# Kernel optimization log

Hardware: AMD Instinct MI355X
Metric: run time of the kernel (lower is better)

Reference implementation:

```python
import jax, jax.numpy as jnp
import numpy as np

NUM_BINS = 8
TAIL = 3.0
MBW = 1e-3  # min_bin_width
MBH = 1e-3  # min_bin_height
MD = 1e-3   # min_derivative
B, C, H, W = 16, 12, 128, 128
COND = C // 3
HID = 64
STEP = 3 * NUM_BINS - 1
OUT = C * STEP


def setup_inputs() -> dict:
    key = jax.random.key(0)
    ks = jax.random.split(key, 8)
    s = lambda k, shape, scale=1.0: jax.random.normal(k, shape, jnp.float32) * scale
    return {
        'x': s(ks[0], (B, C, H, W)),
        'logdet': jnp.zeros((B,), jnp.float32),
        'conditioning': s(ks[1], (B, COND, H, W)),
        'W1': s(ks[2], (HID, C + COND, 3, 3), 0.05), 'b1': jnp.zeros((HID,), jnp.float32),
        'W2': s(ks[3], (HID, HID, 1, 1), 0.05), 'b2': jnp.zeros((HID,), jnp.float32),
        'W3': s(ks[4], (OUT, HID, 3, 3), 0.05), 'b3': jnp.zeros((OUT,), jnp.float32),
    }


def _conv(x, w, b, pad):
    y = jax.lax.conv_general_dilated(x, w, (1, 1), [(pad, pad), (pad, pad)],
                                     dimension_numbers=('NCHW', 'OIHW', 'NCHW'))
    return y + b[None, :, None, None]


def _checker_mask(h, w, parity):
    ii, jj = jnp.meshgrid(jnp.arange(h), jnp.arange(w), indexing='ij')
    m = jnp.where((ii + jj) % 2 == 0, parity, 1 - parity)
    return m.astype(jnp.float32)[None, None]  # (1,1,H,W)


def _rqs_forward(x, uw, uh, ud):
    # x: (B,C,H,W); uw/uh: (...,K); ud: (...,K-1). 'linear' tails, tail_bound=TAIL.
    K = NUM_BINS
    left, right = -TAIL, TAIL
    inside = (x >= left) & (x <= right)
    xc = jnp.clip(x, left, right)

    w = MBW + (1.0 - MBW * K) * jax.nn.softmax(uw, axis=-1)
    cw = jnp.pad(jnp.cumsum(w, -1), [(0, 0)] * (w.ndim - 1) + [(1, 0)])
    cw = (right - left) * cw + left
    cw = cw.at[..., 0].set(left).at[..., -1].set(right)
    w = cw[..., 1:] - cw[..., :-1]

    h = MBH + (1.0 - MBH * K) * jax.nn.softmax(uh, axis=-1)
    ch = jnp.pad(jnp.cumsum(h, -1), [(0, 0)] * (h.ndim - 1) + [(1, 0)])
    ch = (right - left) * ch + left
    ch = ch.at[..., 0].set(left).at[..., -1].set(right)
    h = ch[..., 1:] - ch[..., :-1]

    const = float(np.log(np.expm1(1.0 - MD)))  # boundary derivative -> 1 under linear tails
    udp = jnp.pad(ud, [(0, 0)] * (ud.ndim - 1) + [(1, 1)], constant_values=const)
    d = MD + jax.nn.softplus(udp)  # (...,K+1)

    delta = h / w
    # searchsorted: bin index per element
    idx = jnp.clip(jnp.sum((xc[..., None] >= cw).astype(jnp.int32), -1) - 1, 0, K - 1)[..., None]
    g = lambda t: jnp.take_along_axis(t, idx, axis=-1)[..., 0]

    icw, iw = g(cw), g(w)
    ich, ih = g(ch), g(h)
    idl = g(delta)
    id0 = g(d)
    id1 = g(d[..., 1:])

    theta = (xc - icw) / iw
    t1 = theta * (1.0 - theta)
    num = ih * (idl * theta ** 2 + id0 * t1)
    den = idl + (id0 + id1 - 2.0 * idl) * t1
    y = ich + num / den
    dnum = idl ** 2 * (id1 * theta ** 2 + 2.0 * idl * t1 + id0 * (1.0 - theta) ** 2)
    lad = jnp.log(dnum) - 2.0 * jnp.log(den)
    return jnp.where(inside, y, x), jnp.where(inside, lad, 0.0)


def reference(x, logdet, conditioning, W1, b1, W2, b2, W3, b3):
    mask = _checker_mask(H, W, 0)
    x_frozen = mask * x
    x_active = (1.0 - mask) * x
    z = jnp.concatenate([x_frozen, conditioning], axis=1)
    h1 = jax.nn.relu(_conv(z, W1, b1, 1))
    h2 = jax.nn.relu(_conv(h1, W2, b2, 0))
    params = _conv(h2, W3, b3, 1)  # (B, C*STEP, H, W)
    # all channels at once instead of python loop over C
    p = params.reshape(B, C, STEP, H, W).transpose(0, 1, 3, 4, 2)  # (B,C,H,W,STEP)
    uw = p[..., :NUM_BINS]
    uh = p[..., NUM_BINS:2 * NUM_BINS]
    ud = p[..., 2 * NUM_BINS:]
    y, lad = _rqs_forward(x_active, uw, uh, ud)
    x_out = x_frozen + y  # matches original: frozen part + spline output (no re-masking of y)
    logdet_out = logdet + lad.sum(axis=(1, 2, 3))
    return x_out, logdet_out
```

## Files before the change

### kernel.cpp

```cpp
#include <hip/hip_runtime.h>

#define HW (128*128)

typedef __bf16 bf16x8 __attribute__((ext_vector_type(8)));
typedef float  float4v __attribute__((ext_vector_type(4)));
typedef int    int4v   __attribute__((ext_vector_type(4)));
typedef int    int2v   __attribute__((ext_vector_type(2)));

static __device__ __forceinline__ short f2bf(float f) {
    unsigned u = __float_as_uint(f);
    unsigned r = (u + 0x7FFFu + ((u >> 16) & 1u)) >> 16;
    return (short)(r & 0xFFFFu);
}
static __device__ __forceinline__ int pack2(short a, short b) {
    return (int)((unsigned short)a | ((unsigned)(unsigned short)b << 16));
}
static __device__ __forceinline__ void async_cp16(const void* g, void* l) {
    __builtin_amdgcn_global_load_lds(
        (const __attribute__((address_space(1))) unsigned int*)g,
        (__attribute__((address_space(3))) unsigned int*)l, 16, 0, 0);
}

__global__ __launch_bounds__(256) void prep_weights(
    const float* __restrict__ W1, const float* __restrict__ W2,
    const float* __restrict__ W3,
    short* __restrict__ W1sw, short* __restrict__ W2sw, short* __restrict__ W3sw,
    char* __restrict__ h2p, int4v* __restrict__ zerobuf)
{
    int tid = blockIdx.x * 256 + threadIdx.x;
    int stride = gridDim.x * 256;
    for (int i = tid; i < 5*256*8; i += stride) {
        int e = i & 7, q = (i >> 3) & 255, s = i >> 11;
        int n = q >> 2, c = q & 3;
        int gc = c ^ ((n >> 1) & 3);
        int tap = 2*s + (gc >> 1);
        int ch = (gc & 1)*8 + e;
        float v = 0.f;
        if (tap < 9) {
            int ky = (tap*11) >> 5; int kx = tap - 3*ky;
            v = W1[((n*16 + ch)*3 + ky)*3 + kx];
        }
        W1sw[i] = f2bf(v);
    }
    for (int i = tid; i < 2*256*8; i += stride) {
        int e = i & 7, q = (i >> 3) & 255, s = i >> 11;
        int n = q >> 2, c = q & 3;
        int gc = c ^ ((n >> 1) & 3);
        int k = s*32 + gc*8 + e;
        W2sw[i] = f2bf(W2[n*64 + k]);
    }
    for (int i = tid; i < 9*288*64; i += stride) {
        int e = i & 7;
        int c = (i >> 3) & 7;
        int r = i >> 6;
        int tap = r / 288;
        int n = r - tap*288;
        int ch = n / 24, jj = n - 24*ch;
        int ci = ((c ^ (n & 7)) << 3) + e;
        float v = 0.f;
        if (jj < 23) v = W3[((ch*23 + jj)*64 + ci)*9 + tap];
        W3sw[i] = f2bf(v);
    }
    for (int i = tid; i < 64; i += stride) { int4v zz = {0,0,0,0}; zerobuf[i] = zz; }
    for (int i = tid; i < 16*516*8; i += stride) {
        int cchunk = i & 7, pxi = (i >> 3) % 516, b = i / (516*8);
        int yy, xx;
        if (pxi < 130)      { yy = 0;   xx = pxi; }
        else if (pxi < 260) { yy = 129; xx = pxi - 130; }
        else if (pxi < 388) { yy = pxi - 260 + 1; xx = 0; }
        else                { yy = pxi - 388 + 1; xx = 129; }
        int4v zz = {0,0,0,0};
        *(int4v*)(h2p + (size_t)((b*130 + yy)*130 + xx)*128 + cchunk*16) = zz;
    }
}

__global__ __launch_bounds__(256) void pack_z(
    const float* __restrict__ x, const float* __restrict__ cond,
    short* __restrict__ zp, float* __restrict__ ldslots)
{
    int id = blockIdx.x * 256 + threadIdx.x;
    if (id < 1024) ldslots[id] = 0.f;
    if (id >= 16*130*130) return;
    int b = id / 16900;
    int rem = id - b*16900;
    int yy = rem / 130;
    int xx = rem - yy*130;
    short vs[16];
    #pragma unroll
    for (int c = 0; c < 16; ++c) vs[c] = 0;
    if (yy >= 1 && yy <= 128 && xx >= 1 && xx <= 128) {
        int pix = (yy - 1)*128 + (xx - 1);
        bool frozen = ((yy + xx) & 1) == 1;
        #pragma unroll
        for (int c = 0; c < 12; ++c)
            vs[c] = f2bf(frozen ? x[(b*12 + c)*HW + pix] : 0.f);
        #pragma unroll
        for (int c = 0; c < 4; ++c)
            vs[12 + c] = f2bf(cond[(b*4 + c)*HW + pix]);
    }
    int4v lo = { pack2(vs[0],vs[1]),  pack2(vs[2],vs[3]),
                 pack2(vs[4],vs[5]),  pack2(vs[6],vs[7]) };
    int4v hi = { pack2(vs[8],vs[9]),  pack2(vs[10],vs[11]),
                 pack2(vs[12],vs[13]),pack2(vs[14],vs[15]) };
    *(int4v*)(zp + id*16)     = lo;
    *(int4v*)(zp + id*16 + 8) = hi;
}

__global__ __launch_bounds__(256, 4) void conv12_kernel(
    const char* __restrict__ zp, const char* __restrict__ W1sw,
    const char* __restrict__ W2sw,
    const float* __restrict__ b1, const float* __restrict__ b2,
    const char* __restrict__ zerobuf, char* __restrict__ h2p)
{
    __shared__ __align__(16) char smem[28672];
    int t = threadIdx.x;
    int lane = t & 63, w = t >> 6;
    int l15 = lane & 15, quad = lane >> 4;
    int bid = blockIdx.x;
    int b = bid & 15, y = bid >> 4;
    int chb = (w >> 1) * 32;
    int pxb = (w & 1) * 64;
    unsigned wbase = (unsigned)__builtin_amdgcn_readfirstlane(w << 10);

    int px1 = t >> 2;
    int gc1 = (t & 3) ^ ((px1 >> 1) & 3);
    int tl1 = gc1 >> 1, zoff1 = px1*32 + (gc1 & 1)*16;
    int q2 = t + 256;
    int px2 = q2 >> 2;
    int gc2 = (q2 & 3) ^ ((px2 >> 1) & 3);
    int tl2 = gc2 >> 1, zoff2 = px2*32 + (gc2 & 1)*16;

    int waddr[2], zaddr[4];
    #pragma unroll
    for (int i = 0; i < 2; ++i) {
        int n = chb + i*16 + l15;
        waddr[i] = 8192 + n*64 + ((quad ^ ((n >> 1) & 3)) << 4);
    }
    #pragma unroll
    for (int j = 0; j < 4; ++j) {
        int px = pxb + j*16 + l15;
        zaddr[j] = px*64 + ((quad ^ ((px >> 1) & 3)) << 4);
    }

    const char* zb = zp + (size_t)(b*16900)*32;
    const float4v z4 = {0.f,0.f,0.f,0.f};
    float4v acc[2][4];
    #pragma unroll
    for (int i = 0; i < 2; ++i)
        #pragma unroll
        for (int j = 0; j < 4; ++j) acc[i][j] = z4;

    for (int s = 0; s < 5; ++s) {
        __syncthreads();
        int ta = 2*s + tl1;
        const char* g1;
        if (ta < 9) { int ky = (ta*11) >> 5; int kx = ta - 3*ky;
            g1 = zb + ((y + ky)*130 + kx)*32 + zoff1; }
        else g1 = zerobuf + (lane << 4);
        async_cp16(g1, smem + wbase);
        int tb = 2*s + tl2;
        const char* g2;
        if (tb < 9) { int ky = (tb*11) >> 5; int kx = tb - 3*ky;
            g2 = zb + ((y + ky)*130 + kx)*32 + zoff2; }
        else g2 = zerobuf + (lane << 4);
        async_cp16(g2, smem + 4096 + wbase);
        async_cp16(W1sw + s*4096 + (t << 4), smem + 8192 + wbase);
        __syncthreads();
        bf16x8 aw[2];
        #pragma unroll
        for (int i = 0; i < 2; ++i) aw[i] = *(const bf16x8*)(smem + waddr[i]);
        #pragma unroll
        for (int j = 0; j < 4; ++j) {
            bf16x8 bzv = *(const bf16x8*)(smem + zaddr[j]);
            #pragma unroll
            for (int i = 0; i < 2; ++i)
                acc[i][j] = __builtin_amdgcn_mfma_f32_16x16x32_bf16(aw[i], bzv, acc[i][j], 0, 0, 0);
        }
    }
    {
        #pragma unroll
        for (int i = 0; i < 2; ++i) {
            int ch0 = chb + i*16 + quad*4;
            float bb0 = b1[ch0], bb1 = b1[ch0+1], bb2 = b1[ch0+2], bb3 = b1[ch0+3];
            #pragma unroll
            for (int j = 0; j < 4; ++j) {
                int px = pxb + j*16 + l15;
                short s0 = f2bf(fmaxf(acc[i][j][0] + bb0, 0.f));
                short s1 = f2bf(fmaxf(acc[i][j][1] + bb1, 0.f));
                short s2 = f2bf(fmaxf(acc[i][j][2] + bb2, 0.f));
                short s3 = f2bf(fmaxf(acc[i][j][3] + bb3, 0.f));
                int2v pk = { pack2(s0, s1), pack2(s2, s3) };
                *(int2v*)(smem + 12288 + px*128 + (((ch0 >> 3) ^ (px & 7)) << 4) + ((ch0 & 7) << 1)) = pk;
            }
        }
    }
    float4v acc2[2][4];
    #pragma unroll
    for (int i = 0; i < 2; ++i)
        #pragma unroll
        for (int j = 0; j < 4; ++j) acc2[i][j] = z4;
    for (int s = 0; s < 2; ++s) {
        __syncthreads();
        async_cp16(W2sw + s*4096 + (t << 4), smem + 8192 + wbase);
        __syncthreads();
        bf16x8 aw[2];
        #pragma unroll
        for (int i = 0; i < 2; ++i) aw[i] = *(const bf16x8*)(smem + waddr[i]);
        #pragma unroll
        for (int j = 0; j < 4; ++j) {
            int px = pxb + j*16 + l15;
            bf16x8 bh = *(const bf16x8*)(smem + 12288 + px*128 + (((s*4 + quad) ^ (px & 7)) << 4));
            #pragma unroll
            for (int i = 0; i < 2; ++i)
                acc2[i][j] = __builtin_amdgcn_mfma_f32_16x16x32_bf16(aw[i], bh, acc2[i][j], 0, 0, 0);
        }
    }
    __syncthreads();
    {
        #pragma unroll
        for (int i = 0; i < 2; ++i) {
            int ch0 = chb + i*16 + quad*4;
            float bb0 = b2[ch0], bb1 = b2[ch0+1], bb2 = b2[ch0+2], bb3 = b2[ch0+3];
            #pragma unroll
            for (int j = 0; j < 4; ++j) {
                int px = pxb + j*16 + l15;
                short s0 = f2bf(fmaxf(acc2[i][j][0] + bb0, 0.f));
                short s1 = f2bf(fmaxf(acc2[i][j][1] + bb1, 0.f));
                short s2 = f2bf(fmaxf(acc2[i][j][2] + bb2, 0.f));
                short s3 = f2bf(fmaxf(acc2[i][j][3] + bb3, 0.f));
                int2v pk = { pack2(s0, s1), pack2(s2, s3) };
                *(int2v*)(smem + 12288 + px*128 + (((ch0 >> 3) ^ (px & 7)) << 4) + ((ch0 & 7) << 1)) = pk;
            }
        }
    }
    __syncthreads();
    char* dst = h2p + ((size_t)(b*130 + y + 1)*130 + 1)*128;
    #pragma unroll
    for (int u = 0; u < 4; ++u) {
        int q = t + u*256;
        int px = q >> 3, g = q & 7;
        int4v v = *(const int4v*)(smem + 12288 + px*128 + ((g ^ (px & 7)) << 4));
        *(int4v*)(dst + px*128 + (g << 4)) = v;
    }
}

static __device__ __forceinline__ float rqs_eval(
    const float* __restrict__ pa, float xin, bool frozen, float& ldsum)
{
    float xa = frozen ? 0.f : xin;
    float xf = frozen ? xin : 0.f;
    float xc = fminf(fmaxf(xa, -3.f), 3.f);
    bool inside = (xa >= -3.f) && (xa <= 3.f);

    float mw = pa[0];
    #pragma unroll
    for (int j = 1; j < 8; ++j) mw = fmaxf(mw, pa[j]);
    float ew[8]; float sw = 0.f;
    #pragma unroll
    for (int j = 0; j < 8; ++j) { ew[j] = __expf(pa[j] - mw); sw += ew[j]; }
    float Aw = 0.992f / sw;
    float run = 0.f, cwl = -3.f, icw = -3.f, iwid = 1.f;
    int idx = 0;
    #pragma unroll
    for (int j = 0; j < 8; ++j) {
        float wj = fmaf(Aw, ew[j], 0.001f);
        run += wj;
        float cwr = (j == 7) ? 3.f : fmaf(6.f, run, -3.f);
        if (xc >= cwl) { icw = cwl; iwid = cwr - cwl; idx = j; }
        cwl = cwr;
    }
    float mh = pa[8];
    #pragma unroll
    for (int j = 9; j < 16; ++j) mh = fmaxf(mh, pa[j]);
    float eh[8]; float sh = 0.f;
    #pragma unroll
    for (int j = 0; j < 8; ++j) { eh[j] = __expf(pa[8 + j] - mh); sh += eh[j]; }
    float Ah = 0.992f / sh;
    run = 0.f;
    float chl = -3.f, ich = 0.f, ihei = 1.f;
    #pragma unroll
    for (int j = 0; j < 8; ++j) {
        float hj = fmaf(Ah, eh[j], 0.001f);
        run += hj;
        float chr = (j == 7) ? 3.f : fmaf(6.f, run, -3.f);
        if (j == idx) { ich = chl; ihei = chr - chl; }
        chl = chr;
    }
    float v0 = 0.f, v1 = 0.f;
    bool h0 = false, h1 = false;
    #pragma unroll
    for (int j = 1; j < 8; ++j) {
        float v = pa[15 + j];
        if (j == idx)     { v0 = v; h0 = true; }
        if (j == idx + 1) { v1 = v; h1 = true; }
    }
    float sp0 = (v0 > 15.f) ? v0 : __logf(1.f + __expf(v0));
    float sp1 = (v1 > 15.f) ? v1 : __logf(1.f + __expf(v1));
    float d0 = h0 ? (0.001f + sp0) : 1.f;
    float d1 = h1 ? (0.001f + sp1) : 1.f;

    float dl = ihei / iwid;
    float th = (xc - icw) / iwid;
    float omt = 1.f - th;
    float t1 = th * omt;
    float num = ihei * (dl*th*th + d0*t1);
    float den = dl + (d0 + d1 - 2.f*dl)*t1;
    float yv = ich + num/den;
    float dnum = dl*dl*(d1*th*th + 2.f*dl*t1 + d0*omt*omt);
    float lad = __logf(dnum) - 2.f*__logf(den);

    ldsum += inside ? lad : 0.f;
    return xf + (inside ? yv : xa);
}

__global__ __launch_bounds__(256, 4) void conv3_rqs_kernel(
    const char* __restrict__ h2p, const char* __restrict__ W3sw,
    const float* __restrict__ b3, const float* __restrict__ x,
    float* __restrict__ out, float* __restrict__ ldslots)
{
    __shared__ __align__(16) char smem[28672];
    int t = threadIdx.x;
    int lane = t & 63, w = t >> 6;
    int l15 = lane & 15, quad = lane >> 4;
    int bid = blockIdx.x;
    int b = bid & 15;
    int r0 = bid >> 4;
    int cg = r0 % 3;
    int y = r0 / 3;

    int u = w & 1, v = w >> 1;

    int aaddr[4], baddr[3];
    #pragma unroll
    for (int i = 0; i < 4; ++i) {
        int row = u*64 + i*16 + l15;
        aaddr[i] = row*128 + ((quad ^ (row & 7)) << 4);
    }
    #pragma unroll
    for (int j = 0; j < 3; ++j) {
        int nl = v*48 + j*16 + l15;
        baddr[j] = 16384 + nl*128 + ((quad ^ (nl & 7)) << 4);
    }

    int offA[4];
    #pragma unroll
    for (int r = 0; r < 4; ++r) {
        int q = t + r*256;
        int px = q >> 3, c = q & 7;
        offA[r] = px*128 + ((c ^ (px & 7)) << 4);
    }
    unsigned wbase = (unsigned)__builtin_amdgcn_readfirstlane(w << 10);

    const float4v z4 = {0.f,0.f,0.f,0.f};
    float4v acc[4][3];
    #pragma unroll
    for (int i = 0; i < 4; ++i)
        #pragma unroll
        for (int j = 0; j < 3; ++j) acc[i][j] = z4;

    const char* h2pb = h2p + (size_t)(b*130)*130*128;
    const char* W3b = W3sw + cg*12288;
    for (int tap = 0; tap < 9; ++tap) {
        int ty = (tap*11) >> 5;
        int tx = tap - 3*ty;
        const char* sbA = h2pb + ((y + ty)*130 + tx)*128;
        const char* sbB = W3b + tap*36864;
        __syncthreads();
        #pragma unroll
        for (int r = 0; r < 4; ++r)
            async_cp16(sbA + offA[r], smem + r*4096 + wbase);
        #pragma unroll
        for (int r = 0; r < 3; ++r)
            async_cp16(sbB + r*4096 + (t << 4), smem + 16384 + r*4096 + wbase);
        __syncthreads();
        #pragma unroll
        for (int kh = 0; kh < 2; ++kh) {
            int kx = kh << 6;
            bf16x8 av[4];
            #pragma unroll
            for (int i = 0; i < 4; ++i)
                av[i] = *(const bf16x8*)(smem + (aaddr[i] ^ kx));
            #pragma unroll
            for (int j = 0; j < 3; ++j) {
                bf16x8 bv = *(const bf16x8*)(smem + (baddr[j] ^ kx));
                #pragma unroll
                for (int i = 0; i < 4; ++i)
                    acc[i][j] = __builtin_amdgcn_mfma_f32_16x16x32_bf16(av[i], bv, acc[i][j], 0, 0, 0);
            }
        }
    }
    __syncthreads();

    float* scr = (float*)smem;
    float ldsum = 0.f;
    int pxl = t & 63;
    int chl = t >> 6;
    int c = cg*4 + chl;
    const float* bb3 = b3 + c*23;

    #pragma unroll
    for (int rnd = 0; rnd < 2; ++rnd) {
        if (u == rnd) {
            #pragma unroll
            for (int i = 0; i < 4; ++i)
                #pragma unroll
                for (int j = 0; j < 3; ++j)
                    #pragma unroll
                    for (int r = 0; r < 4; ++r) {
                        int row = i*16 + quad*4 + r;
                        int col = v*48 + j*16 + l15;
                        scr[row*104 + col] = acc[i][j][r];
                    }
        }
        __syncthreads();
        const float* P = scr + pxl*104 + chl*24;
        float pa[23];
        {
            float pr[24];
            *(float4v*)&pr[0]  = *(const float4v*)(P);
            *(float4v*)&pr[4]  = *(const float4v*)(P + 4);
            *(float4v*)&pr[8]  = *(const float4v*)(P + 8);
            *(float4v*)&pr[12] = *(const float4v*)(P + 12);
            *(float4v*)&pr[16] = *(const float4v*)(P + 16);
            *(float4v*)&pr[20] = *(const float4v*)(P + 20);
            #pragma unroll
            for (int j = 0; j < 23; ++j) pa[j] = pr[j] + bb3[j];
        }
        int pxg = rnd*64 + pxl;
        int gidx = ((b*12 + c) << 14) + (y << 7) + pxg;
        float xin = x[gidx];
        bool frozen = ((y + pxg) & 1) == 1;
        out[gidx] = rqs_eval(pa, xin, frozen, ldsum);
        __syncthreads();
    }
    #pragma unroll
    for (int off = 32; off > 0; off >>= 1)
        ldsum += __shfl_down(ldsum, off, 64);
    if (lane == 0) atomicAdd(ldslots + b*64 + (r0 & 63), ldsum);
}

__global__ __launch_bounds__(64) void logdet_reduce(
    const float* __restrict__ ldslots, const float* __restrict__ ld_in,
    float* __restrict__ ldout)
{
    int b = blockIdx.x;
    int lane = threadIdx.x;
    float s = ldslots[b*64 + lane];
    #pragma unroll
    for (int off = 32; off > 0; off >>= 1)
        s += __shfl_down(s, off, 64);
    if (lane == 0) ldout[b] = ld_in[b] + s;
}

extern "C" void kernel_launch(void* const* d_in, const int* in_sizes, int n_in,
                              void* d_out, int out_size, void* d_ws, size_t ws_size,
                              hipStream_t stream)
{
    (void)in_sizes; (void)n_in; (void)out_size; (void)ws_size;
    const float* x    = (const float*)d_in[0];
    const float* ld   = (const float*)d_in[1];
    const float* cond = (const float*)d_in[2];
    const float* W1   = (const float*)d_in[3];
    const float* b1   = (const float*)d_in[4];
    const float* W2   = (const float*)d_in[5];
    const float* b2   = (const float*)d_in[6];
    const float* W3   = (const float*)d_in[7];
    const float* b3   = (const float*)d_in[8];
    float* out = (float*)d_out;
    char* ws = (char*)d_ws;

    short* zp     = (short*)(ws);
    char*  h2p    = ws + 8652800;
    short* W1sw   = (short*)(ws + 43264000);
    short* W2sw   = (short*)(ws + 43284480);
    short* W3sw   = (short*)(ws + 43292672);
    char*  zerob  = ws + 43624448;
    float* ldslots= (float*)(ws + 43625472);
    float* ldout  = out + 12*HW*16;

    prep_weights<<<dim3(256), dim3(256), 0, stream>>>(
        W1, W2, W3, W1sw, W2sw, W3sw, h2p, (int4v*)zerob);
    pack_z<<<dim3(1057), dim3(256), 0, stream>>>(x, cond, zp, ldslots);
    conv12_kernel<<<dim3(2048), dim3(256), 0, stream>>>(
        (const char*)zp, (const char*)W1sw, (const char*)W2sw, b1, b2,
        (const char*)zerob, h2p);
    conv3_rqs_kernel<<<dim3(6144), dim3(256), 0, stream>>>(
        (const char*)h2p, (const char*)W3sw, b3, x, out, ldslots);
    logdet_reduce<<<dim3(16), dim3(64), 0, stream>>>(ldslots, ld, ldout);
}
```

Before: 209.9 us.

## Restructure conv3 to stage all three input rows once and read weights from global

Each block of the conv3+RQS kernel now covers all 288 output channels for one image row instead of a third of them. It uses 384 threads (6 waves, 6 N-tiles each) in place of three blocks of 256 threads per row. The three halo input rows are loaded into LDS once up front, replacing nine per-tap reloads and their barriers. Weights are re-laid out in a plain per-tap/k-half order and fetched straight from global/L2 into registers rather than staged through LDS. This removes redundant input staging and sync, at the cost of larger LDS use (about 51 KB), fewer blocks, and uncached-in-LDS weight reads.

```diff
diff --git a/kernel.cpp b/kernel.cpp
--- a/kernel.cpp
+++ b/kernel.cpp
@@ -24,7 +24,7 @@
 __global__ __launch_bounds__(256) void prep_weights(
     const float* __restrict__ W1, const float* __restrict__ W2,
     const float* __restrict__ W3,
-    short* __restrict__ W1sw, short* __restrict__ W2sw, short* __restrict__ W3sw,
+    short* __restrict__ W1sw, short* __restrict__ W2sw, short* __restrict__ W3g,
     char* __restrict__ h2p, int4v* __restrict__ zerobuf)
 {
     int tid = blockIdx.x * 256 + threadIdx.x;
@@ -49,17 +49,16 @@
         int k = s*32 + gc*8 + e;
         W2sw[i] = f2bf(W2[n*64 + k]);
     }
-    for (int i = tid; i < 9*288*64; i += stride) {
-        int e = i & 7;
-        int c = (i >> 3) & 7;
-        int r = i >> 6;
-        int tap = r / 288;
-        int n = r - tap*288;
+    for (int i = tid; i < 9*2*288*32; i += stride) {
+        int kk = i & 31;
+        int n = (i >> 5) % 288;
+        int tk = i / (288*32);
+        int tap = tk >> 1, kh = tk & 1;
         int ch = n / 24, jj = n - 24*ch;
-        int ci = ((c ^ (n & 7)) << 3) + e;
+        int ci = kh*32 + kk;
         float v = 0.f;
         if (jj < 23) v = W3[((ch*23 + jj)*64 + ci)*9 + tap];
-        W3sw[i] = f2bf(v);
+        W3g[i] = f2bf(v);
     }
     for (int i = tid; i < 64; i += stride) { int4v zz = {0,0,0,0}; zerobuf[i] = zz; }
     for (int i = tid; i < 16*516*8; i += stride) {
@@ -313,76 +312,65 @@
     return xf + (inside ? yv : xa);
 }
 
-__global__ __launch_bounds__(256, 4) void conv3_rqs_kernel(
-    const char* __restrict__ h2p, const char* __restrict__ W3sw,
+__global__ __launch_bounds__(384, 3) void conv3_rqs_kernel(
+    const char* __restrict__ h2p, const char* __restrict__ W3g,
     const float* __restrict__ b3, const float* __restrict__ x,
     float* __restrict__ out, float* __restrict__ ldslots)
 {
-    __shared__ __align__(16) char smem[28672];
+    __shared__ __align__(16) char smem[52224];
     int t = threadIdx.x;
     int lane = t & 63, w = t >> 6;
     int l15 = lane & 15, quad = lane >> 4;
     int bid = blockIdx.x;
     int b = bid & 15;
-    int r0 = bid >> 4;
-    int cg = r0 % 3;
-    int y = r0 / 3;
+    int y = bid >> 4;
 
     int u = w & 1, v = w >> 1;
 
-    int aaddr[4], baddr[3];
-    #pragma unroll
-    for (int i = 0; i < 4; ++i) {
-        int row = u*64 + i*16 + l15;
-        aaddr[i] = row*128 + ((quad ^ (row & 7)) << 4);
-    }
-    #pragma unroll
-    for (int j = 0; j < 3; ++j) {
-        int nl = v*48 + j*16 + l15;
-        baddr[j] = 16384 + nl*128 + ((quad ^ (nl & 7)) << 4);
-    }
-
-    int offA[4];
-    #pragma unroll
-    for (int r = 0; r < 4; ++r) {
-        int q = t + r*256;
-        int px = q >> 3, c = q & 7;
-        offA[r] = px*128 + ((c ^ (px & 7)) << 4);
-    }
-    unsigned wbase = (unsigned)__builtin_amdgcn_readfirstlane(w << 10);
+    const char* h2pb = h2p + (size_t)(b*130)*130*128;
+    #pragma unroll
+    for (int i = 0; i < 9; ++i) {
+        if (i < 8 || w < 3) {
+            int c = t + i*384;
+            int row = c / 1088;
+            int pc = c - row*1088;
+            int px = pc >> 3, sub = pc & 7;
+            int gs = sub ^ (px & 7);
+            const char* g = h2pb + (((y + row)*130 + px) << 7) + (gs << 4);
+            async_cp16(g, smem + i*6144 + (w << 10));
+        }
+    }
+    __syncthreads();
 
     const float4v z4 = {0.f,0.f,0.f,0.f};
-    float4v acc[4][3];
+    float4v acc[4][6];
     #pragma unroll
     for (int i = 0; i < 4; ++i)
         #pragma unroll
-        for (int j = 0; j < 3; ++j) acc[i][j] = z4;
-
-    const char* h2pb = h2p + (size_t)(b*130)*130*128;
-    const char* W3b = W3sw + cg*12288;
+        for (int j = 0; j < 6; ++j) acc[i][j] = z4;
+
+    const char* W3base = W3g;
+    int laneoff = l15*64 + quad*16;
+    int pxb0 = u*64 + l15;
+
     for (int tap = 0; tap < 9; ++tap) {
         int ty = (tap*11) >> 5;
         int tx = tap - 3*ty;
-        const char* sbA = h2pb + ((y + ty)*130 + tx)*128;
-        const char* sbB = W3b + tap*36864;
-        __syncthreads();
-        #pragma unroll
-        for (int r = 0; r < 4; ++r)
-            async_cp16(sbA + offA[r], smem + r*4096 + wbase);
-        #pragma unroll
-        for (int r = 0; r < 3; ++r)
-            async_cp16(sbB + r*4096 + (t << 4), smem + 16384 + r*4096 + wbase);
-        __syncthreads();
+        int arow = ty * 17408;
         #pragma unroll
         for (int kh = 0; kh < 2; ++kh) {
-            int kx = kh << 6;
             bf16x8 av[4];
             #pragma unroll
-            for (int i = 0; i < 4; ++i)
-                av[i] = *(const bf16x8*)(smem + (aaddr[i] ^ kx));
-            #pragma unroll
-            for (int j = 0; j < 3; ++j) {
-                bf16x8 bv = *(const bf16x8*)(smem + (baddr[j] ^ kx));
+            for (int i = 0; i < 4; ++i) {
+                int px = pxb0 + i*16 + tx;
+                av[i] = *(const bf16x8*)(smem + arow + (px << 7)
+                         + ((((kh << 2) + quad) ^ (px & 7)) << 4));
+            }
+            const char* bseg = W3base
+                + ((((tap << 1) + kh)*288 + v*96) << 6) + laneoff;
+            #pragma unroll
+            for (int j = 0; j < 6; ++j) {
+                bf16x8 bv = *(const bf16x8*)(bseg + (j << 10));
                 #pragma unroll
                 for (int i = 0; i < 4; ++i)
                     acc[i][j] = __builtin_amdgcn_mfma_f32_16x16x32_bf16(av[i], bv, acc[i][j], 0, 0, 0);
@@ -393,27 +381,25 @@
 
     float* scr = (float*)smem;
     float ldsum = 0.f;
-    int pxl = t & 63;
-    int chl = t >> 6;
-    int c = cg*4 + chl;
-    const float* bb3 = b3 + c*23;
-
-    #pragma unroll
-    for (int rnd = 0; rnd < 2; ++rnd) {
-        if (u == rnd) {
-            #pragma unroll
-            for (int i = 0; i < 4; ++i)
+    int pxl = t & 31;
+    int ch = t >> 5;
+    const float* bb3 = b3 + ch*23;
+
+    #pragma unroll
+    for (int q = 0; q < 4; ++q) {
+        if (u == (q >> 1)) {
+            #pragma unroll
+            for (int i2 = 0; i2 < 2; ++i2) {
+                int i = ((q & 1) << 1) + i2;
                 #pragma unroll
-                for (int j = 0; j < 3; ++j)
+                for (int j = 0; j < 6; ++j)
                     #pragma unroll
-                    for (int r = 0; r < 4; ++r) {
-                        int row = i*16 + quad*4 + r;
-                        int col = v*48 + j*16 + l15;
-                        scr[row*104 + col] = acc[i][j][r];
-                    }
-        }
-        __syncthreads();
-        const float* P = scr + pxl*104 + chl*24;
+                    for (int r = 0; r < 4; ++r)
+                        scr[(i2*16 + quad*4 + r)*292 + v*96 + j*16 + l15] = acc[i][j][r];
+            }
+        }
+        __syncthreads();
+        const float* P = scr + pxl*292 + ch*24;
         float pa[23];
         {
             float pr[24];
@@ -426,8 +412,8 @@
             #pragma unroll
             for (int j = 0; j < 23; ++j) pa[j] = pr[j] + bb3[j];
         }
-        int pxg = rnd*64 + pxl;
-        int gidx = ((b*12 + c) << 14) + (y << 7) + pxg;
+        int pxg = (q << 5) + pxl;
+        int gidx = ((b*12 + ch) << 14) + (y << 7) + pxg;
         float xin = x[gidx];
         bool frozen = ((y + pxg) & 1) == 1;
         out[gidx] = rqs_eval(pa, xin, frozen, ldsum);
@@ -436,7 +422,7 @@
     #pragma unroll
     for (int off = 32; off > 0; off >>= 1)
         ldsum += __shfl_down(ldsum, off, 64);
-    if (lane == 0) atomicAdd(ldslots + b*64 + (r0 & 63), ldsum);
+    if (lane == 0) atomicAdd(ldslots + b*64 + (y & 63), ldsum);
 }
 
 __global__ __launch_bounds__(64) void logdet_reduce(
@@ -473,18 +459,18 @@
     char*  h2p    = ws + 8652800;
     short* W1sw   = (short*)(ws + 43264000);
     short* W2sw   = (short*)(ws + 43284480);
-    short* W3sw   = (short*)(ws + 43292672);
+    short* W3g    = (short*)(ws + 43292672);
     char*  zerob  = ws + 43624448;
     float* ldslots= (float*)(ws + 43625472);
     float* ldout  = out + 12*HW*16;
 
     prep_weights<<<dim3(256), dim3(256), 0, stream>>>(
-        W1, W2, W3, W1sw, W2sw, W3sw, h2p, (int4v*)zerob);
+        W1, W2, W3, W1sw, W2sw, W3g, h2p, (int4v*)zerob);
     pack_z<<<dim3(1057), dim3(256), 0, stream>>>(x, cond, zp, ldslots);
     conv12_kernel<<<dim3(2048), dim3(256), 0, stream>>>(
         (const char*)zp, (const char*)W1sw, (const char*)W2sw, b1, b2,
         (const char*)zerob, h2p);
-    conv3_rqs_kernel<<<dim3(6144), dim3(256), 0, stream>>>(
-        (const char*)h2p, (const char*)W3sw, b3, x, out, ldslots);
+    conv3_rqs_kernel<<<dim3(2048), dim3(384), 0, stream>>>(
+        (const char*)h2p, (const char*)W3g, b3, x, out, ldslots);
     logdet_reduce<<<dim3(16), dim3(64), 0, stream>>>(ldslots, ld, ldout);
 }
```

Measured after the change: 259.5 us. 23.6% more time.
